# Kernel tuning notes

Measured on AMD Instinct MI355X. Metric: run time of the kernel, lower is better.

## Reference

```python
import jax, jax.numpy as jnp
import numpy as np

A = -0.75  # torch bicubic cubic-convolution coefficient

def _cubic_k(t):
    at = jnp.abs(t)
    return jnp.where(at <= 1, (A + 2) * at**3 - (A + 3) * at**2 + 1,
           jnp.where(at < 2, A * at**3 - 5 * A * at**2 + 8 * A * at - 4 * A, 0.0))

def _resize_last(x, out_size):
    # bicubic, align_corners=True, along last axis
    in_size = x.shape[-1]
    pos = jnp.arange(out_size, dtype=x.dtype) * ((in_size - 1) / (out_size - 1))
    i0 = jnp.floor(pos).astype(jnp.int32)
    frac = pos - i0
    offs = jnp.arange(-1, 3, dtype=jnp.int32)                    # 4 taps
    idx = jnp.clip(i0[None] + offs[:, None], 0, in_size - 1)     # [4, out]
    w = _cubic_k(frac[None] - offs[:, None].astype(x.dtype))     # [4, out]
    g = x[..., idx]                                              # [..., 4, out]
    return jnp.einsum('...ko,ko->...o', g, w)

def bicubic(x, H, W):
    x = _resize_last(x, W)
    x = jnp.swapaxes(_resize_last(jnp.swapaxes(x, -1, -2), H), -1, -2)
    return x

def conv(x, w, b):
    y = jax.lax.conv_general_dilated(x, w, (1, 1), 'SAME',
                                     dimension_numbers=('NCHW', 'OIHW', 'NCHW'))
    return y + b[None, :, None, None]

def pool(x):
    return jax.lax.reduce_window(x, -jnp.inf, jax.lax.max, (1, 1, 2, 2), (1, 1, 2, 2), 'VALID')

def extract(x, ws, bs):
    # feat1: vgg19 features[:2]
    x1 = jax.nn.relu(conv(x, ws[0], bs[0]))
    # feat2: vgg19 features[2:18]
    h = jax.nn.relu(conv(x1, ws[1], bs[1])); h = pool(h)
    h = jax.nn.relu(conv(h, ws[2], bs[2]))
    h = jax.nn.relu(conv(h, ws[3], bs[3])); h = pool(h)
    for i in range(4, 8):
        h = jax.nn.relu(conv(h, ws[i], bs[i]))
    h = bicubic(h, x1.shape[-2], x1.shape[-1])
    return jnp.concatenate([x1, h], axis=1)  # [B, 320, H, W]

def normalizer(f1, f2):
    B, C = f1.shape[:2]
    a = f1.reshape(B, C, -1)
    b = f2.reshape(B, C, -1)
    xc = jnp.concatenate([a, b], axis=-1)
    mean = xc.mean(-1, keepdims=True)
    std = xc.mean(-1, keepdims=True)  # faithful to original source bug: std = mean
    a = (a - mean) / (std + 1e-8)
    b = (b - mean) / (std + 1e-8)
    return a.reshape(f1.shape), b.reshape(f2.shape)

_CHANS = [(3, 64), (64, 64), (64, 128), (128, 128), (128, 256), (256, 256), (256, 256), (256, 256)]

def setup_inputs() -> dict:
    key = jax.random.key(0)
    ks = jax.random.split(key, 20)
    inp = {}
    for i, (ci, co) in enumerate(_CHANS):
        inp[f'w{i}'] = jax.random.normal(ks[i], (co, ci, 3, 3), jnp.float32) * np.sqrt(2.0 / (ci * 9))
        inp[f'b{i}'] = jnp.zeros((co,), jnp.float32)
    inp['x_ref'] = jax.random.normal(ks[16], (2, 3, 96, 96), jnp.float32)
    inp['x_template'] = jax.random.normal(ks[17], (2, 3, 48, 48), jnp.float32)
    inp['coef_ref'] = jnp.float32(1.0)
    inp['coef_tmp'] = jnp.float32(1.0)
    return inp

def reference(x_ref, x_template, coef_ref, coef_tmp,
              w0, b0, w1, b1, w2, b2, w3, b3, w4, b4, w5, b5, w6, b6, w7, b7):
    ws = [w0, w1, w2, w3, w4, w5, w6, w7]
    bs = [b0, b1, b2, b3, b4, b5, b6, b7]
    fref = extract(x_ref, ws, bs)
    ftem = extract(x_template, ws, bs)
    fref, ftem = normalizer(fref, ftem)
    B, C, m, n = fref.shape
    _, _, p, q = ftem.shape
    dist = jnp.einsum('bcmn,bcpq->bmnpq', fref, ftem).reshape(B, m * n, p * q)
    conf_ref = jax.nn.softmax(coef_ref * dist, axis=-2)
    conf_tmp = jax.nn.softmax(coef_tmp * dist, axis=-1)
    confidence = jnp.sqrt(conf_ref * conf_tmp)
    vals, _ = jax.lax.top_k(confidence, 10)
    values = vals.mean(-1, keepdims=True).reshape(B, m, n, 1)
    return values
```

## Files before the change

### kernel.cpp

```cpp
#include <hip/hip_runtime.h>
#include <math.h>

#define CK_A (-0.75f)

typedef __attribute__((ext_vector_type(8))) short bf16x8;
typedef __attribute__((ext_vector_type(4))) float f32x4;

struct CImg { const float* in; float* out; int H, W, tiles; long inBS, outBS, sStride; };

__device__ __forceinline__ float cubicw(float t){
  float at = fabsf(t);
  float at2 = at*at, at3 = at2*at;
  if (at <= 1.f) return (CK_A+2.f)*at3 - (CK_A+3.f)*at2 + 1.f;
  if (at < 2.f)  return CK_A*at3 - 5.f*CK_A*at2 + 8.f*CK_A*at - 4.f*CK_A;
  return 0.f;
}

__device__ __forceinline__ unsigned short f2bf_rne(float f){
  unsigned int u = __float_as_uint(f);
  unsigned int r = (u + 0x7fffu + ((u>>16)&1u)) >> 16;
  return (unsigned short)r;
}
__device__ __forceinline__ float bf2f(unsigned short h){
  return __uint_as_float(((unsigned int)h)<<16);
}

__device__ __forceinline__ void merge_ms(float& m, float& s, float m2, float s2){
  float M = fmaxf(m, m2);
  s = s*__expf(m - M) + s2*__expf(m2 - M);
  m = M;
}

#define MFB(a,b,c) __builtin_amdgcn_mfma_f32_16x16x32_bf16(a,b,c,0,0,0)

typedef const __attribute__((address_space(1))) unsigned int* gp1_t;
typedef __attribute__((address_space(3))) unsigned int* lp3_t;
__device__ __forceinline__ void dma16(const void* g, void* l){
  __builtin_amdgcn_global_load_lds((gp1_t)g, (lp3_t)l, 16, 0, 0);
}

__global__ __launch_bounds__(256) void conv0_d(CImg A, CImg B,
    const float* __restrict__ w, const float* __restrict__ bias){
  bool isA = (int)blockIdx.x < A.tiles;
  const float* in = isA ? A.in : B.in;
  float* out = isA ? A.out : B.out;
  int H = isA ? A.H : B.H, W = isA ? A.W : B.W;
  long inBS = isA ? A.inBS : B.inBS, outBS = isA ? A.outBS : B.outBS;
  int tile = isA ? blockIdx.x : blockIdx.x - A.tiles;
  int tilesX = (W + 15) >> 4;
  int tx0 = (tile % tilesX) << 4, ty0 = (tile / tilesX) << 4;
  int cob = blockIdx.y * 4;
  int b = blockIdx.z;
  int lx = threadIdx.x & 15, ly = threadIdx.x >> 4;
  __shared__ float tile_s[3][18][20];
  float acc[4] = {0.f,0.f,0.f,0.f};
  const float* inb = in + (long)b*inBS;
  int ox = tx0+lx, oy = ty0+ly;

  for (int idx = threadIdx.x; idx < 3*324; idx += 256){
    int cl = idx/324, rem = idx - cl*324;
    int r = rem/18, c = rem - r*18;
    int gy = ty0 + r - 1, gx = tx0 + c - 1;
    const float* ic = inb + (long)cl*H*W;
    tile_s[cl][r][c] = (gy>=0 && gy<H && gx>=0 && gx<W) ? ic[(long)gy*W+gx] : 0.f;
  }
  __syncthreads();
  #pragma unroll
  for (int cl=0; cl<3; cl++){
    float t00=tile_s[cl][ly+0][lx+0], t01=tile_s[cl][ly+0][lx+1], t02=tile_s[cl][ly+0][lx+2];
    float t10=tile_s[cl][ly+1][lx+0], t11=tile_s[cl][ly+1][lx+1], t12=tile_s[cl][ly+1][lx+2];
    float t20=tile_s[cl][ly+2][lx+0], t21=tile_s[cl][ly+2][lx+1], t22=tile_s[cl][ly+2][lx+2];
    #pragma unroll
    for (int j=0;j<4;j++){
      const float* wp = w + ((long)(cob+j)*3 + cl)*9;
      float a = acc[j];
      a = fmaf(t00, wp[0], a); a = fmaf(t01, wp[1], a); a = fmaf(t02, wp[2], a);
      a = fmaf(t10, wp[3], a); a = fmaf(t11, wp[4], a); a = fmaf(t12, wp[5], a);
      a = fmaf(t20, wp[6], a); a = fmaf(t21, wp[7], a); a = fmaf(t22, wp[8], a);
      acc[j] = a;
    }
  }
  if (ox < W && oy < H){
    #pragma unroll
    for (int j=0;j<4;j++){
      float v = fmaxf(acc[j] + bias[cob+j], 0.f);
      out[(long)b*outBS + (long)(cob+j)*H*W + (long)oy*W + ox] = v;
    }
  }
}

__global__ void prep_w_all(const float* __restrict__ w1, const float* __restrict__ w2,
                           const float* __restrict__ w3, const float* __restrict__ w4,
                           const float* __restrict__ w5, const float* __restrict__ w6,
                           const float* __restrict__ w7, unsigned short* __restrict__ wp){
  const int ciT[7] = {64,64,128,128,256,256,256};
  const int coT[7] = {64,128,128,256,256,256,256};
  int l = blockIdx.y;
  const float* w = l==0?w1: l==1?w2: l==2?w3: l==3?w4: l==4?w5: l==5?w6: w7;
  long offv = 0;
  for (int i=0;i<7;i++){ if (i<l) offv += 9L*ciT[i]*coT[i]*2; }
  long total = 9L*ciT[l]*coT[l]*2;
  long e = (long)blockIdx.x*256 + threadIdx.x;
  if (e >= total) return;
  int CI = ciT[l], CO = coT[l];
  int j = (int)(e & 7);
  int lane = (int)((e>>3) & 63);
  int h = (int)((e>>9) & 1);
  long rem = e >> 10;
  int G = CO >> 4, KC = CI >> 5;
  int g = (int)(rem % G); long q = rem / G;
  int kc = (int)(q % KC); int o = (int)(q / KC);
  int co = (g<<4) + (lane & 15);
  int ci = (kc<<5) + ((lane>>4)<<3) + j;
  float v = w[((long)co*CI + ci)*9 + o];
  unsigned short hi = f2bf_rne(v);
  wp[offv + e] = (h==0) ? hi : f2bf_rne(v - bf2f(hi));
}

union AB { bf16x8 v; uint4 u; };

__global__ __launch_bounds__(256) void conv_mfma_d(
    CImg A, CImg B, const unsigned short* __restrict__ Wp,
    const float* __restrict__ bias, int CI, int CO, int nci, int S)
{
  bool isA = (int)blockIdx.x < A.tiles;
  const float* in = isA ? A.in : B.in;
  float* out = isA ? A.out : B.out;
  int H = isA ? A.H : B.H, W = isA ? A.W : B.W;
  long inBS = isA ? A.inBS : B.inBS, outBS = isA ? A.outBS : B.outBS;
  long sStride = isA ? A.sStride : B.sStride;
  int tile = isA ? blockIdx.x : blockIdx.x - A.tiles;

  int HW = H*W;
  int tilesX = (W+7)>>3;
  int tx0 = (tile % tilesX)<<3, ty0 = (tile / tilesX)<<3;
  int cobase = blockIdx.y << 6;
  int s = blockIdx.z % S, b = blockIdx.z / S;
  int tid = threadIdx.x, lane = tid & 63, wid = tid>>6;
  int wm = wid>>1, wn = wid&1;
  int KC = CI>>5, G = CO>>4;
  __shared__ __align__(16) unsigned short Bth[4000];
  __shared__ __align__(16) unsigned short Btl[4000];
  const float* inb = in + (long)b*inBS;

  int sofs[13]; int sla[13];
  #pragma unroll
  for (int i=0;i<13;i++){
    int e = tid + i*256;
    int cidx = e / 100, pix = e - cidx*100;
    int hy = pix/10, hx = pix - hy*10;
    int gy = ty0 - 1 + hy, gx = tx0 - 1 + hx;
    bool v = (gy>=0) && (gy<H) && (gx>=0) && (gx<W);
    sofs[i] = v ? (cidx*HW + gy*W + gx) : -1;
    sla[i] = pix*40 + cidx;
  }

  int n15 = lane & 15;
  int klane8 = (lane>>4)<<3;
  int p0 = wn*32 + n15;
  int base0 = ((p0>>3)*10 + (p0&7))*40 + klane8;
  int p1 = p0 + 16;
  int base1 = ((p1>>3)*10 + (p1&7))*40 + klane8;
  int g0 = (cobase>>4) + wm*2;

  f32x4 acc[2][2];
  #pragma unroll
  for (int i=0;i<2;i++)
    #pragma unroll
    for (int j=0;j<2;j++) acc[i][j] = (f32x4){0.f,0.f,0.f,0.f};

  int nkc = nci >> 5;
  for (int kk=0; kk<nkc; kk++){
    int ci0 = s*nci + (kk<<5);
    __syncthreads();
    #pragma unroll
    for (int i=0;i<12;i++){
      float v = (sofs[i] >= 0) ? inb[(long)ci0*HW + sofs[i]] : 0.f;
      unsigned short h = f2bf_rne(v);
      Bth[sla[i]] = h;
      Btl[sla[i]] = f2bf_rne(v - bf2f(h));
    }
    if (tid < 128){
      float v = (sofs[12] >= 0) ? inb[(long)ci0*HW + sofs[12]] : 0.f;
      unsigned short h = f2bf_rne(v);
      Bth[sla[12]] = h;
      Btl[sla[12]] = f2bf_rne(v - bf2f(h));
    }
    __syncthreads();
    int kc = ci0 >> 5;
    const unsigned short* wpb = Wp + (long)kc*G*1024 + (long)lane*8;
    #pragma unroll
    for (int o=0;o<9;o++){
      const int dy = o/3, dx = o - dy*3;
      const int sh = (dy*10+dx)*40;
      const unsigned short* wo = wpb + (long)o*KC*G*1024;
      AB a0h,a0l,a1h,a1l, b0h,b0l,b1h,b1l;
      a0h.u = *(const uint4*)(wo + (long)g0*1024);
      a0l.u = *(const uint4*)(wo + (long)g0*1024 + 512);
      a1h.u = *(const uint4*)(wo + (long)(g0+1)*1024);
      a1l.u = *(const uint4*)(wo + (long)(g0+1)*1024 + 512);
      b0h.v = *(const bf16x8*)&Bth[base0 + sh];
      b0l.v = *(const bf16x8*)&Btl[base0 + sh];
      b1h.v = *(const bf16x8*)&Bth[base1 + sh];
      b1l.v = *(const bf16x8*)&Btl[base1 + sh];
      acc[0][0] = MFB(a0h.v, b0l.v, acc[0][0]);
      acc[0][0] = MFB(a0l.v, b0h.v, acc[0][0]);
      acc[0][0] = MFB(a0h.v, b0h.v, acc[0][0]);
      acc[0][1] = MFB(a0h.v, b1l.v, acc[0][1]);
      acc[0][1] = MFB(a0l.v, b1h.v, acc[0][1]);
      acc[0][1] = MFB(a0h.v, b1h.v, acc[0][1]);
      acc[1][0] = MFB(a1h.v, b0l.v, acc[1][0]);
      acc[1][0] = MFB(a1l.v, b0h.v, acc[1][0]);
      acc[1][0] = MFB(a1h.v, b0h.v, acc[1][0]);
      acc[1][1] = MFB(a1h.v, b1l.v, acc[1][1]);
      acc[1][1] = MFB(a1l.v, b1h.v, acc[1][1]);
      acc[1][1] = MFB(a1h.v, b1h.v, acc[1][1]);
    }
  }

  float* outp = out + (long)s*sStride + (long)b*outBS;
  #pragma unroll
  for (int ng=0; ng<2; ng++){
    int p = wn*32 + ng*16 + n15;
    int gy = ty0 + (p>>3), gx = tx0 + (p&7);
    bool ok = (gy<H) && (gx<W);
    #pragma unroll
    for (int mg=0; mg<2; mg++){
      #pragma unroll
      for (int r=0;r<4;r++){
        if (ok){
          int co = cobase + wm*32 + mg*16 + ((lane>>4)<<2) + r;
          float v = acc[mg][ng][r];
          if (bias) v = fmaxf(v + bias[co], 0.f);
          outp[(long)co*HW + (long)gy*W + gx] = v;
        }
      }
    }
  }
}

__global__ void reduce_d(const float* __restrict__ pA, const float* __restrict__ pB,
                         const float* __restrict__ bias,
                         float* __restrict__ oA, float* __restrict__ oB,
                         int S, long sStrA, long sStrB, int CO, int HWa, int HWb,
                         long oBSa, long oBSb){
  int img = blockIdx.y;
  const float* part = img ? pB : pA;
  float* out = img ? oB : oA;
  int HW = img ? HWb : HWa;
  long sStride = img ? sStrB : sStrA;
  long outBS = img ? oBSb : oBSa;
  long tot = 2L*CO*HW;
  long e = (long)blockIdx.x*256 + threadIdx.x;
  if (e >= tot) return;
  long b = e / ((long)CO*HW);
  long r = e - b*(long)CO*HW;
  float v = 0.f;
  for (int s=0;s<S;s++) v += part[(long)s*sStride + e];
  int co = (int)(r / HW);
  out[b*outBS + r] = fmaxf(v + bias[co], 0.f);
}

__global__ void maxpool2_d(const float* __restrict__ inA, float* __restrict__ outA, long NCa, int HiA, int WiA,
                           const float* __restrict__ inB, float* __restrict__ outB, long NCb, int HiB, int WiB){
  const float* in = blockIdx.y ? inB : inA;
  float* out = blockIdx.y ? outB : outA;
  long NC = blockIdx.y ? NCb : NCa;
  int Hi = blockIdx.y ? HiB : HiA, Wi = blockIdx.y ? WiB : WiA;
  int Ho = Hi>>1, Wo = Wi>>1;
  long total = NC * Ho * Wo;
  long idx = (long)blockIdx.x*256 + threadIdx.x;
  if (idx >= total) return;
  int x = (int)(idx % Wo); long t = idx / Wo; int y = (int)(t % Ho); long nc = t / Ho;
  const float* p = in + (nc*Hi + 2*y)*(long)Wi + 2*x;
  out[idx] = fmaxf(fmaxf(p[0], p[1]), fmaxf(p[Wi], p[Wi+1]));
}

__global__ __launch_bounds__(256) void bicubic_d(
    const float* __restrict__ inA, float* __restrict__ outA,
    const float* __restrict__ inB, float* __restrict__ outB){
  int c = blockIdx.x;
  int img = blockIdx.y >> 1, b = blockIdx.y & 1;
  const float* in = img ? inB : inA;
  float* out = img ? outB : outA;
  int Hin = img ? 12 : 24, Win = Hin, Hout = img ? 48 : 96, Wout = Hout;
  long inBS = img ? 256L*144 : 256L*576;
  long outBS = img ? 320L*2304 : 320L*9216;
  __shared__ float s[576];
  const float* ip = in + (long)b*inBS + (long)c*Hin*Win;
  float* op = out + (long)b*outBS + (long)c*Hout*Wout;
  int n = Hin*Win;
  for (int i = threadIdx.x; i < n; i += 256) s[i] = ip[i];
  __syncthreads();
  float scy = (float)((double)(Hin-1)/(double)(Hout-1));
  float scx = scy;
  int total = Hout*Wout;
  for (int idx = threadIdx.x; idx < total; idx += 256){
    int ox = idx % Wout, oy = idx / Wout;
    float py = oy * scy, px = ox * scx;
    float iy0f = floorf(py), ix0f = floorf(px);
    int iy0 = (int)iy0f, ix0 = (int)ix0f;
    float fy = py - iy0f, fx = px - ix0f;
    float wy[4], wx[4]; int xs[4], ys[4];
    #pragma unroll
    for (int t=0;t<4;t++){
      wy[t] = cubicw(fy - (float)(t-1));
      wx[t] = cubicw(fx - (float)(t-1));
      ys[t] = min(max(iy0 + t - 1, 0), Hin-1);
      xs[t] = min(max(ix0 + t - 1, 0), Win-1);
    }
    float acc = 0.f;
    #pragma unroll
    for (int i=0;i<4;i++){
      const float* row = &s[ys[i]*Win];
      float rs = wx[0]*row[xs[0]] + wx[1]*row[xs[1]] + wx[2]*row[xs[2]] + wx[3]*row[xs[3]];
      acc = fmaf(wy[i], rs, acc);
    }
    op[idx] = acc;
  }
}

__global__ __launch_bounds__(256) void mean_k(const float* __restrict__ fR, const float* __restrict__ fT, float* __restrict__ mean){
  int c = blockIdx.x % 320, b = blockIdx.x / 320;
  const float* a = fR + ((long)b*320+c)*9216L;
  const float* t = fT + ((long)b*320+c)*2304L;
  float s = 0.f;
  for (int i=threadIdx.x;i<9216;i+=256) s += a[i];
  for (int i=threadIdx.x;i<2304;i+=256) s += t[i];
  __shared__ float sm[4];
  for (int o=32;o;o>>=1) s += __shfl_down(s,o);
  int lane = threadIdx.x & 63, wv = threadIdx.x >> 6;
  if (lane==0) sm[wv] = s;
  __syncthreads();
  if (threadIdx.x==0) mean[b*320+c] = (sm[0]+sm[1]+sm[2]+sm[3]) * (1.f/11520.f);
}

__global__ __launch_bounds__(256) void split_bf16_d(const float* __restrict__ fR, const float* __restrict__ fT,
    const float* __restrict__ mean,
    unsigned short* __restrict__ AhR, unsigned short* __restrict__ AlR,
    unsigned short* __restrict__ BhT, unsigned short* __restrict__ BlT){
  bool isR = blockIdx.x < 288;
  const float* feat = isR ? fR : fT;
  unsigned short* oh = isR ? AhR : BhT;
  unsigned short* ol = isR ? AlR : BlT;
  int P = isR ? 9216 : 2304;
  int m0 = (isR ? blockIdx.x : blockIdx.x - 288) * 32;
  int b = blockIdx.y;
  __shared__ unsigned int t[32][321];
  int ml = threadIdx.x & 31, kq = threadIdx.x >> 5;
  const float* fp = feat + (long)b*320*P + m0 + ml;
  for (int k = kq*40; k < kq*40+40; k++){
    float mu = mean[b*320+k];
    float v = (fp[(long)k*P] - mu) / (mu + 1e-8f);
    unsigned short h = f2bf_rne(v);
    unsigned short l = f2bf_rne(v - bf2f(h));
    t[ml][k] = ((unsigned int)h<<16) | l;
  }
  __syncthreads();
  long base = ((long)b*P + m0)*320;
  for (int idx = threadIdx.x; idx < 32*320; idx += 256){
    int m = idx/320, k = idx - m*320;
    unsigned int p = t[m][k];
    oh[base + (long)m*320 + k] = (unsigned short)(p>>16);
    ol[base + (long)m*320 + k] = (unsigned short)(p & 0xffffu);
  }
}

__global__ __launch_bounds__(256) void gemm_mfma(
    const unsigned short* __restrict__ Ah, const unsigned short* __restrict__ Al,
    const unsigned short* __restrict__ Bh, const unsigned short* __restrict__ Bl,
    float* __restrict__ D, const float* __restrict__ coefr,
    float* __restrict__ pm, float* __restrict__ ps){
  const int N = 2304, K = 320;
  int n0 = blockIdx.x*128, m0 = blockIdx.y*128;
  __shared__ __align__(16) unsigned short SF[16384];
  int tid = threadIdx.x, lane = tid & 63, wid = tid >> 6;
  int wm = wid >> 1, wn = wid & 1;
  int n15 = lane & 15, q = lane >> 4;
  f32x4 acc[4][4];
  #pragma unroll
  for (int i=0;i<4;i++)
    #pragma unroll
    for (int j=0;j<4;j++) acc[i][j] = (f32x4){0.f,0.f,0.f,0.f};

  const unsigned short* srcB[8];
  #pragma unroll
  for (int i=0;i<8;i++){
    int li = i*256 + tid;
    int rem = li & 1023;
    int row = rem >> 3, sg = rem & 7;
    int seg = sg ^ (row & 7);
    if (li < 1024) srcB[i] = ((seg<4) ? Ah : Al) + (long)(m0+row)*K + (seg&3)*8;
    else           srcB[i] = ((seg<4) ? Bh : Bl) + (long)(n0+row)*K + (seg&3)*8;
  }

  int aH[4], aL[4], bH[4], bL[4];
  #pragma unroll
  for (int g=0; g<4; g++){
    int ra = wm*64 + g*16 + n15;
    int rb = wn*64 + g*16 + n15;
    aH[g] = ra*64 + (( q   ) ^ (ra&7))*8;
    aL[g] = ra*64 + ((q+4) ^ (ra&7))*8;
    bH[g] = 8192 + rb*64 + (( q   ) ^ (rb&7))*8;
    bL[g] = 8192 + rb*64 + ((q+4) ^ (rb&7))*8;
  }

  for (int k0=0; k0<K; k0+=32){
    __syncthreads();
    #pragma unroll
    for (int i=0;i<8;i++){
      dma16(srcB[i] + k0, (void*)&SF[((i<<8) + (wid<<6))<<3]);
    }
    __syncthreads();

    AB af[2][4], bf[2][4];
    #pragma unroll
    for (int g=0; g<4; g++){
      af[0][g].v = *(const bf16x8*)&SF[aH[g]];
      af[1][g].v = *(const bf16x8*)&SF[aL[g]];
      bf[0][g].v = *(const bf16x8*)&SF[bH[g]];
      bf[1][g].v = *(const bf16x8*)&SF[bL[g]];
    }
    #pragma unroll
    for (int mg=0; mg<4; mg++)
      #pragma unroll
      for (int ng=0; ng<4; ng++){
        acc[mg][ng] = MFB(af[0][mg].v, bf[1][ng].v, acc[mg][ng]);
        acc[mg][ng] = MFB(af[1][mg].v, bf[0][ng].v, acc[mg][ng]);
        acc[mg][ng] = MFB(af[0][mg].v, bf[0][ng].v, acc[mg][ng]);
      }
  }
  __syncthreads();

  #pragma unroll
  for (int mg=0; mg<4; mg++)
    #pragma unroll
    for (int ng=0; ng<4; ng++){
      int col = n0 + wn*64 + ng*16 + n15;
      #pragma unroll
      for (int r=0;r<4;r++){
        int rowv = m0 + wm*64 + mg*16 + q*4 + r;
        D[(long)rowv*N + col] = acc[mg][ng][r];
      }
    }

  float cr = *coefr;
  float* red = (float*)&SF[0];
  float pmv[4], psv[4];
  #pragma unroll
  for (int ng=0; ng<4; ng++){
    float m = -INFINITY;
    #pragma unroll
    for (int mg=0; mg<4; mg++)
      #pragma unroll
      for (int r=0;r<4;r++) m = fmaxf(m, cr*acc[mg][ng][r]);
    float s = 0.f;
    #pragma unroll
    for (int mg=0; mg<4; mg++)
      #pragma unroll
      for (int r=0;r<4;r++) s += __expf(cr*acc[mg][ng][r] - m);
    #pragma unroll
    for (int o=16;o<64;o<<=1){
      float m2 = __shfl_xor(m,o), s2 = __shfl_xor(s,o);
      merge_ms(m,s,m2,s2);
    }
    pmv[ng]=m; psv[ng]=s;
  }
  if (q==0){
    #pragma unroll
    for (int ng=0; ng<4; ng++){
      int cl = wn*64 + ng*16 + lane;
      red[wm*128 + cl] = pmv[ng];
      red[256 + wm*128 + cl] = psv[ng];
    }
  }
  __syncthreads();
  if (wm==0 && q==0){
    #pragma unroll
    for (int ng=0; ng<4; ng++){
      int cl = wn*64 + ng*16 + lane;
      float m = pmv[ng], s = psv[ng];
      merge_ms(m, s, red[128+cl], red[384+cl]);
      pm[(long)blockIdx.y*2304 + n0 + cl] = m;
      ps[(long)blockIdx.y*2304 + n0 + cl] = s;
    }
  }
}

__global__ void colstat_merge(const float* __restrict__ pm, const float* __restrict__ ps,
                              float* __restrict__ qcol){
  int idx = blockIdx.x*256 + threadIdx.x;
  if (idx >= 2304) return;
  float m=-INFINITY, s=0.f;
  for (int k=0;k<72;k++) merge_ms(m, s, pm[(long)k*2304+idx], ps[(long)k*2304+idx]);
  qcol[idx] = 0.5f*m + 0.5f*__logf(s);
}

__global__ __launch_bounds__(256) void conf_topk_f(const float* __restrict__ D,
    const float* __restrict__ coefr, const float* __restrict__ coeft,
    const float* __restrict__ qcol, float* __restrict__ outp){
  int m = blockIdx.x;
  const float* drow = D + (long)m*2304;
  int tid = threadIdx.x, lane = tid & 63, wv = tid >> 6;
  float ct = *coeft, cr = *coefr;
  float v[9], tv[9];
  #pragma unroll
  for (int i=0;i<9;i++){ v[i] = drow[tid + i*256]; tv[i] = ct * v[i]; }

  __shared__ float sred[8];
  __shared__ unsigned int cand[40];

  float mx = tv[0];
  #pragma unroll
  for (int i=1;i<9;i++) mx = fmaxf(mx, tv[i]);
  #pragma unroll
  for (int o=1;o<64;o<<=1) mx = fmaxf(mx, __shfl_xor(mx, o));
  if (lane==0) sred[wv] = mx;
  __syncthreads();
  mx = fmaxf(fmaxf(sred[0],sred[1]), fmaxf(sred[2],sred[3]));
  float s = 0.f;
  #pragma unroll
  for (int i=0;i<9;i++) s += __expf(tv[i]-mx);
  #pragma unroll
  for (int o=1;o<64;o<<=1) s += __shfl_xor(s, o);
  if (lane==0) sred[4+wv] = s;
  __syncthreads();
  float rs = sred[4]+sred[5]+sred[6]+sred[7];
  float rho = 0.5f*mx + 0.5f*__logf(rs);
  float hc = 0.5f*(cr+ct);

  unsigned int key[9];
  #pragma unroll
  for (int i=0;i<9;i++){
    int n = i*256 + tid;
    float t = fmaf(hc, v[i], -qcol[n]);
    unsigned int b = __float_as_uint(t);
    b ^= (b >> 31) ? 0xFFFFFFFFu : 0x80000000u;
    key[i] = (b & 0xFFFFF000u) | (unsigned)n;
  }

  for (int t10=0; t10<10; t10++){
    unsigned int lb = key[0];
    #pragma unroll
    for (int i=1;i<9;i++) lb = lb > key[i] ? lb : key[i];
    unsigned int wb = lb;
    #pragma unroll
    for (int o=1;o<64;o<<=1){
      unsigned int x = (unsigned int)__shfl_xor((int)wb, o);
      wb = wb > x ? wb : x;
    }
    if (lane==0) cand[wv*10 + t10] = wb;
    #pragma unroll
    for (int i=0;i<9;i++) if (key[i]==wb) key[i]=0;
  }
  __syncthreads();

  if (wv == 0){
    unsigned int k = (lane < 40) ? cand[lane] : 0u;
    int sel = -1;
    for (int t10=0; t10<10; t10++){
      unsigned int wb = k;
      #pragma unroll
      for (int o=1;o<64;o<<=1){
        unsigned int x = (unsigned int)__shfl_xor((int)wb, o);
        wb = wb > x ? wb : x;
      }
      if (k == wb) k = 0;
      if (lane == t10) sel = (int)(wb & 0xFFFu);
    }
    float c = 0.f;
    if (sel >= 0){
      float t = fmaf(hc, drow[sel], -qcol[sel]);
      c = __expf(t - rho);
    }
    #pragma unroll
    for (int o=1;o<64;o<<=1) c += __shfl_xor(c, o);
    if (lane == 0) outp[m] = c * 0.1f;
  }
}

extern "C" void kernel_launch(void* const* d_in, const int* in_sizes, int n_in,
                              void* d_out, int out_size, void* d_ws, size_t ws_size,
                              hipStream_t stream) {
  const float *W[8], *Bp[8], *xr, *xt, *cr, *ct;
  if (in_sizes[0] == 1728){
    for (int i=0;i<8;i++){ W[i]=(const float*)d_in[2*i]; Bp[i]=(const float*)d_in[2*i+1]; }
    xr=(const float*)d_in[16]; xt=(const float*)d_in[17];
    cr=(const float*)d_in[18]; ct=(const float*)d_in[19];
  } else {
    xr=(const float*)d_in[0]; xt=(const float*)d_in[1];
    cr=(const float*)d_in[2]; ct=(const float*)d_in[3];
    for (int i=0;i<8;i++){ W[i]=(const float*)d_in[4+2*i]; Bp[i]=(const float*)d_in[5+2*i]; }
  }

  const int convCI[8] = {3,64,64,128,128,256,256,256};
  const int convCO[8] = {64,64,128,128,256,256,256,256};
  long wpoff[8]; long wtot = 0;
  for (int l=1;l<8;l++){ wpoff[l] = wtot; wtot += 9L*convCI[l]*convCO[l]*2; }

  float* ws = (float*)d_ws;
  long off = 0;
  auto alloc = [&](long nfl){ float* p = ws + off; off += (nfl + 63) & ~63L; return p; };
  float* featR = alloc(2L*320*9216);
  float* featT = alloc(2L*320*2304);
  float* meanb = alloc(640);
  float* pm    = alloc(72L*2304);
  float* ps    = alloc(72L*2304);
  float* qcol  = alloc(2304);
  unsigned short* wp = (unsigned short*)alloc((wtot+1)/2);
  float* scratch = alloc(9216L*2304);
  if ((size_t)(off*4) > ws_size) return;

  unsigned short* AhR = (unsigned short*)alloc((2L*9216*320 + 1)/2);
  unsigned short* AlR = (unsigned short*)alloc((2L*9216*320 + 1)/2);
  unsigned short* BhT = (unsigned short*)alloc((2L*2304*320 + 1)/2);
  unsigned short* BlT = (unsigned short*)alloc((2L*2304*320 + 1)/2);
  if ((size_t)(off*4) > ws_size) return;

  float* rA = scratch;
  float* rB = rA + 1179648;
  float* rC = rB + 294912;
  float* rD = rC + 589824;
  float* rE = rD + 589824;
  float* rF = rE + 147456;
  float* rG = rF + 294912;
  float* a2 = rG + 294912;
  float* b2 = a2 + 294912;
  float* c2 = b2 + 73728;
  float* d2 = c2 + 147456;
  float* e2 = d2 + 147456;
  float* f2 = e2 + 36864;
  float* g2 = f2 + 73728;
  float* tPR = g2 + 73728;
  float* tPT = tPR + 1179648;
  float* dist = scratch;

  auto mkimg = [](const float* in, float* out, int H, int Wd, int tiles,
                  long inBS, long outBS, long sStr){
    CImg c; c.in=in; c.out=out; c.H=H; c.W=Wd; c.tiles=tiles;
    c.inBS=inBS; c.outBS=outBS; c.sStride=sStr; return c;
  };

  prep_w_all<<<dim3(4608,7), 256, 0, stream>>>(W[1],W[2],W[3],W[4],W[5],W[6],W[7], wp);

  {
    CImg A = mkimg(xr, featR, 96,96, 36, 3L*9216, 320L*9216, 0);
    CImg B = mkimg(xt, featT, 48,48, 9, 3L*2304, 320L*2304, 0);
    conv0_d<<<dim3(45,16,2), 256, 0, stream>>>(A, B, W[0], Bp[0]);
  }
  {
    CImg A = mkimg(featR, rA, 96,96, 144, 320L*9216, 64L*9216, 0);
    CImg B = mkimg(featT, a2, 48,48, 36, 320L*2304, 64L*2304, 0);
    conv_mfma_d<<<dim3(180,1,2), 256, 0, stream>>>(A,B, wp+wpoff[1], Bp[1], 64,64,64,1);
  }
  maxpool2_d<<<dim3(1152,2), 256, 0, stream>>>(rA,rB,128,96,96, a2,b2,128,48,48);
  {
    CImg A = mkimg(rB, tPR, 48,48, 36, 64L*2304, 128L*2304, 589824);
    CImg B = mkimg(b2, tPT, 24,24, 9, 64L*576, 128L*576, 147456);
    conv_mfma_d<<<dim3(45,2,4), 256, 0, stream>>>(A,B, wp+wpoff[2], nullptr, 64,128,32,2);
    reduce_d<<<dim3(2304,2), 256, 0, stream>>>(tPR,tPT,Bp[2], rC,c2, 2, 589824,147456, 128, 2304,576, 128L*2304, 128L*576);
  }
  {
    CImg A = mkimg(rC, tPR, 48,48, 36, 128L*2304, 128L*2304, 589824);
    CImg B = mkimg(c2, tPT, 24,24, 9, 128L*576, 128L*576, 147456);
    conv_mfma_d<<<dim3(45,2,4), 256, 0, stream>>>(A,B, wp+wpoff[3], nullptr, 128,128,64,2);
    reduce_d<<<dim3(2304,2), 256, 0, stream>>>(tPR,tPT,Bp[3], rD,d2, 2, 589824,147456, 128, 2304,576, 128L*2304, 128L*576);
  }
  maxpool2_d<<<dim3(576,2), 256, 0, stream>>>(rD,rE,256,48,48, d2,e2,256,24,24);
  {
    CImg A = mkimg(rE, tPR, 24,24, 9, 128L*576, 256L*576, 294912);
    CImg B = mkimg(e2, tPT, 12,12, 4, 128L*144, 256L*144, 73728);
    conv_mfma_d<<<dim3(13,4,8), 256, 0, stream>>>(A,B, wp+wpoff[4], nullptr, 128,256,32,4);
    reduce_d<<<dim3(1152,2), 256, 0, stream>>>(tPR,tPT,Bp[4], rF,f2, 4, 294912,73728, 256, 576,144, 256L*576, 256L*144);
  }
  const float* inR[3] = {rF, rG, rF};  float* outR[3] = {rG, rF, rG};
  const float* inT[3] = {f2, g2, f2};  float* outT[3] = {g2, f2, g2};
  for (int i=0;i<3;i++){
    int l = 5+i;
    CImg A = mkimg(inR[i], tPR, 24,24, 9, 256L*576, 256L*576, 294912);
    CImg B = mkimg(inT[i], tPT, 12,12, 4, 256L*144, 256L*144, 73728);
    conv_mfma_d<<<dim3(13,4,8), 256, 0, stream>>>(A,B, wp+wpoff[l], nullptr, 256,256,64,4);
    reduce_d<<<dim3(1152,2), 256, 0, stream>>>(tPR,tPT,Bp[l], outR[i],outT[i], 4, 294912,73728, 256, 576,144, 256L*576, 256L*144);
  }
  bicubic_d<<<dim3(256,4), 256, 0, stream>>>(rG, featR + 64L*9216, g2, featT + 64L*2304);

  mean_k<<<640, 256, 0, stream>>>(featR, featT, meanb);
  split_bf16_d<<<dim3(360,2), 256, 0, stream>>>(featR, featT, meanb, AhR, AlR, BhT, BlT);

  for (int b=0; b<2; b++){
    gemm_mfma<<<dim3(18,72), 256, 0, stream>>>(
        AhR + (long)b*9216*320, AlR + (long)b*9216*320,
        BhT + (long)b*2304*320, BlT + (long)b*2304*320, dist, cr, pm, ps);
    colstat_merge<<<dim3(9), 256, 0, stream>>>(pm, ps, qcol);
    conf_topk_f<<<dim3(9216), 256, 0, stream>>>(dist, cr, ct, qcol, (float*)d_out + (long)b*9216);
  }
}
```

Baseline: 455.9 us.

## Store intermediate activations pre-split as packed bf16 hi/lo pairs

Every producer (conv0, the fused-bias conv, reduce) now writes activations as a packed 32-bit word holding the bf16 hi and lo parts. Conv input staging then only unpacks bits instead of running two bf16 conversions per element on every load. Maxpool compares the unpacked values and forwards the packed word, and bicubic unpacks on load. This removes repeated split work across the tiles and channel chunks that reread each input, at the cost of an extra packed output buffer for conv0 and a larger scratch layout.

```diff
diff --git a/kernel.cpp b/kernel.cpp
--- a/kernel.cpp
+++ b/kernel.cpp
@@ -6,7 +6,7 @@
 typedef __attribute__((ext_vector_type(8))) short bf16x8;
 typedef __attribute__((ext_vector_type(4))) float f32x4;
 
-struct CImg { const float* in; float* out; int H, W, tiles; long inBS, outBS, sStride; };
+struct CImg { const void* in; void* out; int H, W, tiles; long inBS, outBS, sStride; };
 
 __device__ __forceinline__ float cubicw(float t){
   float at = fabsf(t);
@@ -24,6 +24,14 @@
 __device__ __forceinline__ float bf2f(unsigned short h){
   return __uint_as_float(((unsigned int)h)<<16);
 }
+__device__ __forceinline__ unsigned pack_bf(float v){
+  unsigned short h = f2bf_rne(v);
+  unsigned short l = f2bf_rne(v - bf2f(h));
+  return ((unsigned)h<<16) | (unsigned)l;
+}
+__device__ __forceinline__ float unpack_bf(unsigned p){
+  return bf2f((unsigned short)(p>>16)) + bf2f((unsigned short)(p&0xffffu));
+}
 
 __device__ __forceinline__ void merge_ms(float& m, float& s, float m2, float s2){
   float M = fmaxf(m, m2);
@@ -40,10 +48,12 @@
 }
 
 __global__ __launch_bounds__(256) void conv0_d(CImg A, CImg B,
-    const float* __restrict__ w, const float* __restrict__ bias){
+    const float* __restrict__ w, const float* __restrict__ bias,
+    unsigned* __restrict__ pOutA, unsigned* __restrict__ pOutB){
   bool isA = (int)blockIdx.x < A.tiles;
-  const float* in = isA ? A.in : B.in;
-  float* out = isA ? A.out : B.out;
+  const float* in = (const float*)(isA ? A.in : B.in);
+  float* out = (float*)(isA ? A.out : B.out);
+  unsigned* pout = isA ? pOutA : pOutB;
   int H = isA ? A.H : B.H, W = isA ? A.W : B.W;
   long inBS = isA ? A.inBS : B.inBS, outBS = isA ? A.outBS : B.outBS;
   int tile = isA ? blockIdx.x : blockIdx.x - A.tiles;
@@ -56,12 +66,13 @@
   float acc[4] = {0.f,0.f,0.f,0.f};
   const float* inb = in + (long)b*inBS;
   int ox = tx0+lx, oy = ty0+ly;
+  int HW = H*W;
 
   for (int idx = threadIdx.x; idx < 3*324; idx += 256){
     int cl = idx/324, rem = idx - cl*324;
     int r = rem/18, c = rem - r*18;
     int gy = ty0 + r - 1, gx = tx0 + c - 1;
-    const float* ic = inb + (long)cl*H*W;
+    const float* ic = inb + (long)cl*HW;
     tile_s[cl][r][c] = (gy>=0 && gy<H && gx>=0 && gx<W) ? ic[(long)gy*W+gx] : 0.f;
   }
   __syncthreads();
@@ -84,7 +95,9 @@
     #pragma unroll
     for (int j=0;j<4;j++){
       float v = fmaxf(acc[j] + bias[cob+j], 0.f);
-      out[(long)b*outBS + (long)(cob+j)*H*W + (long)oy*W + ox] = v;
+      long pix = (long)(cob+j)*HW + (long)oy*W + ox;
+      out[(long)b*outBS + pix] = v;
+      pout[(long)b*64*HW + pix] = pack_bf(v);
     }
   }
 }
@@ -124,8 +137,8 @@
     const float* __restrict__ bias, int CI, int CO, int nci, int S)
 {
   bool isA = (int)blockIdx.x < A.tiles;
-  const float* in = isA ? A.in : B.in;
-  float* out = isA ? A.out : B.out;
+  const unsigned* in = (const unsigned*)(isA ? A.in : B.in);
+  void* outv = isA ? A.out : B.out;
   int H = isA ? A.H : B.H, W = isA ? A.W : B.W;
   long inBS = isA ? A.inBS : B.inBS, outBS = isA ? A.outBS : B.outBS;
   long sStride = isA ? A.sStride : B.sStride;
@@ -141,7 +154,7 @@
   int KC = CI>>5, G = CO>>4;
   __shared__ __align__(16) unsigned short Bth[4000];
   __shared__ __align__(16) unsigned short Btl[4000];
-  const float* inb = in + (long)b*inBS;
+  const unsigned* inb = in + (long)b*inBS;
 
   int sofs[13]; int sla[13];
   #pragma unroll
@@ -175,16 +188,14 @@
     __syncthreads();
     #pragma unroll
     for (int i=0;i<12;i++){
-      float v = (sofs[i] >= 0) ? inb[(long)ci0*HW + sofs[i]] : 0.f;
-      unsigned short h = f2bf_rne(v);
-      Bth[sla[i]] = h;
-      Btl[sla[i]] = f2bf_rne(v - bf2f(h));
+      unsigned p = (sofs[i] >= 0) ? inb[(long)ci0*HW + sofs[i]] : 0u;
+      Bth[sla[i]] = (unsigned short)(p>>16);
+      Btl[sla[i]] = (unsigned short)(p & 0xffffu);
     }
     if (tid < 128){
-      float v = (sofs[12] >= 0) ? inb[(long)ci0*HW + sofs[12]] : 0.f;
-      unsigned short h = f2bf_rne(v);
-      Bth[sla[12]] = h;
-      Btl[sla[12]] = f2bf_rne(v - bf2f(h));
+      unsigned p = (sofs[12] >= 0) ? inb[(long)ci0*HW + sofs[12]] : 0u;
+      Bth[sla[12]] = (unsigned short)(p>>16);
+      Btl[sla[12]] = (unsigned short)(p & 0xffffu);
     }
     __syncthreads();
     int kc = ci0 >> 5;
@@ -218,7 +229,6 @@
     }
   }
 
-  float* outp = out + (long)s*sStride + (long)b*outBS;
   #pragma unroll
   for (int ng=0; ng<2; ng++){
     int p = wn*32 + ng*16 + n15;
@@ -230,9 +240,15 @@
       for (int r=0;r<4;r++){
         if (ok){
           int co = cobase + wm*32 + mg*16 + ((lane>>4)<<2) + r;
+          long idx = (long)co*HW + (long)gy*W + gx;
           float v = acc[mg][ng][r];
-          if (bias) v = fmaxf(v + bias[co], 0.f);
-          outp[(long)co*HW + (long)gy*W + gx] = v;
+          if (bias){
+            unsigned* outp = (unsigned*)outv + (long)b*outBS;
+            outp[idx] = pack_bf(fmaxf(v + bias[co], 0.f));
+          } else {
+            float* outp = (float*)outv + (long)s*sStride + (long)b*outBS;
+            outp[idx] = v;
+          }
         }
       }
     }
@@ -241,12 +257,12 @@
 
 __global__ void reduce_d(const float* __restrict__ pA, const float* __restrict__ pB,
                          const float* __restrict__ bias,
-                         float* __restrict__ oA, float* __restrict__ oB,
+                         unsigned* __restrict__ oA, unsigned* __restrict__ oB,
                          int S, long sStrA, long sStrB, int CO, int HWa, int HWb,
                          long oBSa, long oBSb){
   int img = blockIdx.y;
   const float* part = img ? pB : pA;
-  float* out = img ? oB : oA;
+  unsigned* out = img ? oB : oA;
   int HW = img ? HWb : HWa;
   long sStride = img ? sStrB : sStrA;
   long outBS = img ? oBSb : oBSa;
@@ -258,13 +274,13 @@
   float v = 0.f;
   for (int s=0;s<S;s++) v += part[(long)s*sStride + e];
   int co = (int)(r / HW);
-  out[b*outBS + r] = fmaxf(v + bias[co], 0.f);
-}
-
-__global__ void maxpool2_d(const float* __restrict__ inA, float* __restrict__ outA, long NCa, int HiA, int WiA,
-                           const float* __restrict__ inB, float* __restrict__ outB, long NCb, int HiB, int WiB){
-  const float* in = blockIdx.y ? inB : inA;
-  float* out = blockIdx.y ? outB : outA;
+  out[b*outBS + r] = pack_bf(fmaxf(v + bias[co], 0.f));
+}
+
+__global__ void maxpool2_d(const unsigned* __restrict__ inA, unsigned* __restrict__ outA, long NCa, int HiA, int WiA,
+                           const unsigned* __restrict__ inB, unsigned* __restrict__ outB, long NCb, int HiB, int WiB){
+  const unsigned* in = blockIdx.y ? inB : inA;
+  unsigned* out = blockIdx.y ? outB : outA;
   long NC = blockIdx.y ? NCb : NCa;
   int Hi = blockIdx.y ? HiB : HiA, Wi = blockIdx.y ? WiB : WiA;
   int Ho = Hi>>1, Wo = Wi>>1;
@@ -272,25 +288,31 @@
   long idx = (long)blockIdx.x*256 + threadIdx.x;
   if (idx >= total) return;
   int x = (int)(idx % Wo); long t = idx / Wo; int y = (int)(t % Ho); long nc = t / Ho;
-  const float* p = in + (nc*Hi + 2*y)*(long)Wi + 2*x;
-  out[idx] = fmaxf(fmaxf(p[0], p[1]), fmaxf(p[Wi], p[Wi+1]));
+  const unsigned* p = in + (nc*Hi + 2*y)*(long)Wi + 2*x;
+  unsigned c0=p[0], c1=p[1], c2=p[Wi], c3=p[Wi+1];
+  float v0=unpack_bf(c0), v1=unpack_bf(c1), v2=unpack_bf(c2), v3=unpack_bf(c3);
+  unsigned best=c0; float bv=v0;
+  if (v1>bv){bv=v1;best=c1;}
+  if (v2>bv){bv=v2;best=c2;}
+  if (v3>bv){bv=v3;best=c3;}
+  out[idx] = best;
 }
 
 __global__ __launch_bounds__(256) void bicubic_d(
-    const float* __restrict__ inA, float* __restrict__ outA,
-    const float* __restrict__ inB, float* __restrict__ outB){
+    const unsigned* __restrict__ inA, float* __restrict__ outA,
+    const unsigned* __restrict__ inB, float* __restrict__ outB){
   int c = blockIdx.x;
   int img = blockIdx.y >> 1, b = blockIdx.y & 1;
-  const float* in = img ? inB : inA;
+  const unsigned* in = img ? inB : inA;
   float* out = img ? outB : outA;
   int Hin = img ? 12 : 24, Win = Hin, Hout = img ? 48 : 96, Wout = Hout;
   long inBS = img ? 256L*144 : 256L*576;
   long outBS = img ? 320L*2304 : 320L*9216;
   __shared__ float s[576];
-  const float* ip = in + (long)b*inBS + (long)c*Hin*Win;
+  const unsigned* ip = in + (long)b*inBS + (long)c*Hin*Win;
   float* op = out + (long)b*outBS + (long)c*Hout*Wout;
   int n = Hin*Win;
-  for (int i = threadIdx.x; i < n; i += 256) s[i] = ip[i];
+  for (int i = threadIdx.x; i < n; i += 256) s[i] = unpack_bf(ip[i]);
   __syncthreads();
   float scy = (float)((double)(Hin-1)/(double)(Hout-1));
   float scx = scy;
@@ -352,9 +374,7 @@
   for (int k = kq*40; k < kq*40+40; k++){
     float mu = mean[b*320+k];
     float v = (fp[(long)k*P] - mu) / (mu + 1e-8f);
-    unsigned short h = f2bf_rne(v);
-    unsigned short l = f2bf_rne(v - bf2f(h));
-    t[ml][k] = ((unsigned int)h<<16) | l;
+    t[ml][k] = pack_bf(v);
   }
   __syncthreads();
   long base = ((long)b*P + m0)*320;
@@ -617,25 +637,27 @@
   unsigned short* BlT = (unsigned short*)alloc((2L*2304*320 + 1)/2);
   if ((size_t)(off*4) > ws_size) return;
 
-  float* rA = scratch;
-  float* rB = rA + 1179648;
-  float* rC = rB + 294912;
-  float* rD = rC + 589824;
-  float* rE = rD + 589824;
-  float* rF = rE + 147456;
-  float* rG = rF + 294912;
-  float* a2 = rG + 294912;
-  float* b2 = a2 + 294912;
-  float* c2 = b2 + 73728;
-  float* d2 = c2 + 147456;
-  float* e2 = d2 + 147456;
-  float* f2 = e2 + 36864;
-  float* g2 = f2 + 73728;
-  float* tPR = g2 + 73728;
+  unsigned* pc0R = (unsigned*)scratch;
+  unsigned* pc0T = pc0R + 1179648;
+  unsigned* rA   = pc0T + 294912;
+  unsigned* rB   = rA + 1179648;
+  unsigned* rC   = rB + 294912;
+  unsigned* rD   = rC + 589824;
+  unsigned* rE   = rD + 589824;
+  unsigned* rF   = rE + 147456;
+  unsigned* rG   = rF + 294912;
+  unsigned* a2   = rG + 294912;
+  unsigned* b2   = a2 + 294912;
+  unsigned* c2   = b2 + 73728;
+  unsigned* d2   = c2 + 147456;
+  unsigned* e2   = d2 + 147456;
+  unsigned* f2   = e2 + 36864;
+  unsigned* g2   = f2 + 73728;
+  float* tPR = (float*)(g2 + 73728);
   float* tPT = tPR + 1179648;
   float* dist = scratch;
 
-  auto mkimg = [](const float* in, float* out, int H, int Wd, int tiles,
+  auto mkimg = [](const void* in, void* out, int H, int Wd, int tiles,
                   long inBS, long outBS, long sStr){
     CImg c; c.in=in; c.out=out; c.H=H; c.W=Wd; c.tiles=tiles;
     c.inBS=inBS; c.outBS=outBS; c.sStride=sStr; return c;
@@ -646,11 +668,11 @@
   {
     CImg A = mkimg(xr, featR, 96,96, 36, 3L*9216, 320L*9216, 0);
     CImg B = mkimg(xt, featT, 48,48, 9, 3L*2304, 320L*2304, 0);
-    conv0_d<<<dim3(45,16,2), 256, 0, stream>>>(A, B, W[0], Bp[0]);
+    conv0_d<<<dim3(45,16,2), 256, 0, stream>>>(A, B, W[0], Bp[0], pc0R, pc0T);
   }
   {
-    CImg A = mkimg(featR, rA, 96,96, 144, 320L*9216, 64L*9216, 0);
-    CImg B = mkimg(featT, a2, 48,48, 36, 320L*2304, 64L*2304, 0);
+    CImg A = mkimg(pc0R, rA, 96,96, 144, 64L*9216, 64L*9216, 0);
+    CImg B = mkimg(pc0T, a2, 48,48, 36, 64L*2304, 64L*2304, 0);
     conv_mfma_d<<<dim3(180,1,2), 256, 0, stream>>>(A,B, wp+wpoff[1], Bp[1], 64,64,64,1);
   }
   maxpool2_d<<<dim3(1152,2), 256, 0, stream>>>(rA,rB,128,96,96, a2,b2,128,48,48);
@@ -673,8 +695,8 @@
     conv_mfma_d<<<dim3(13,4,8), 256, 0, stream>>>(A,B, wp+wpoff[4], nullptr, 128,256,32,4);
     reduce_d<<<dim3(1152,2), 256, 0, stream>>>(tPR,tPT,Bp[4], rF,f2, 4, 294912,73728, 256, 576,144, 256L*576, 256L*144);
   }
-  const float* inR[3] = {rF, rG, rF};  float* outR[3] = {rG, rF, rG};
-  const float* inT[3] = {f2, g2, f2};  float* outT[3] = {g2, f2, g2};
+  const unsigned* inR[3] = {rF, rG, rF};  unsigned* outR[3] = {rG, rF, rG};
+  const unsigned* inT[3] = {f2, g2, f2};  unsigned* outT[3] = {g2, f2, g2};
   for (int i=0;i<3;i++){
     int l = 5+i;
     CImg A = mkimg(inR[i], tPR, 24,24, 9, 256L*576, 256L*576, 294912);
```

After: 455.2 us. No clear change (-0.1%).
